# Kernel tuning notes

Hardware: AMD Instinct MI355X
Metric: run time of the kernel (lower is better)

Reference implementation:

```python
import jax, jax.numpy as jnp
import numpy as np

N, E = 50000, 600000
IN, H, O, HEADS = 14, 128, 64, 4
EPS = 1e-5


def layer_norm(x, g, b):
    m = jnp.mean(x, axis=-1, keepdims=True)
    v = jnp.mean((x - m) ** 2, axis=-1, keepdims=True)
    return (x - m) * jax.lax.rsqrt(v + EPS) * g + b


def sage_conv(x, src, dst, W_l, b_l, W_r):
    # mean aggregation of source messages at destination, then lin_l(agg)+lin_r(x)
    s = jax.ops.segment_sum(x[src], dst, num_segments=N)            # [N,H]
    cnt = jax.ops.segment_sum(jnp.ones((src.shape[0],), x.dtype), dst, num_segments=N)
    agg = s / jnp.maximum(cnt, 1.0)[:, None]
    return agg @ W_l + b_l + x @ W_r


def gat_conv(x, src, dst, W_g, att_src, att_dst, b_g):
    # PyG GATConv with add_self_loops=True, heads=4, concat=False -> head mean
    loop = jnp.arange(N, dtype=src.dtype)
    s2 = jnp.concatenate([src, loop])
    d2 = jnp.concatenate([dst, loop])
    h = (x @ W_g).reshape(N, HEADS, O)                               # [N,4,64]
    a_s = jnp.sum(h * att_src, axis=-1)                              # [N,4]
    a_d = jnp.sum(h * att_dst, axis=-1)
    e = jax.nn.leaky_relu(a_s[s2] + a_d[d2], negative_slope=0.2)     # [E+N,4]
    m = jax.ops.segment_max(e, d2, num_segments=N)
    ex = jnp.exp(e - m[d2])
    den = jax.ops.segment_sum(ex, d2, num_segments=N)
    alpha = ex / den[d2]                                             # edge softmax
    out = jax.ops.segment_sum(h[s2] * alpha[..., None], d2, num_segments=N)
    return jnp.mean(out, axis=1) + b_g                               # [N,64]


def setup_inputs() -> dict:
    key = jax.random.key(0)
    ks = jax.random.split(key, 18)
    sc = 0.05
    return {
        'x': jax.random.normal(ks[0], (N, IN), jnp.float32),
        'edge_index': jax.random.randint(ks[1], (2, E), 0, N, dtype=jnp.int64),
        'W_in': jax.random.normal(ks[2], (IN, H), jnp.float32) * sc,
        'b_in': jnp.zeros((H,), jnp.float32),
        'W1_l': jax.random.normal(ks[3], (H, H), jnp.float32) * sc,
        'b1': jnp.zeros((H,), jnp.float32),
        'W1_r': jax.random.normal(ks[4], (H, H), jnp.float32) * sc,
        'g1': jnp.ones((H,), jnp.float32),
        'be1': jnp.zeros((H,), jnp.float32),
        'W2_l': jax.random.normal(ks[5], (H, H), jnp.float32) * sc,
        'b2': jnp.zeros((H,), jnp.float32),
        'W2_r': jax.random.normal(ks[6], (H, H), jnp.float32) * sc,
        'g2': jnp.ones((H,), jnp.float32),
        'be2': jnp.zeros((H,), jnp.float32),
        'W_g': jax.random.normal(ks[7], (H, HEADS * O), jnp.float32) * sc,
        'att_src': jax.random.normal(ks[8], (HEADS, O), jnp.float32) * sc,
        'att_dst': jax.random.normal(ks[9], (HEADS, O), jnp.float32) * sc,
        'b_g': jnp.zeros((O,), jnp.float32),
        'g3': jnp.ones((O,), jnp.float32),
        'be3': jnp.zeros((O,), jnp.float32),
    }


def reference(x, edge_index, W_in, b_in, W1_l, b1, W1_r, g1, be1,
              W2_l, b2, W2_r, g2, be2, W_g, att_src, att_dst, b_g, g3, be3):
    src, dst = edge_index[0], edge_index[1]
    h = jax.nn.relu(x @ W_in + b_in)                 # input_proj + relu (dropout: eval)
    # layer 0: SAGE + LN + relu + residual
    h_res = h
    h = jax.nn.relu(layer_norm(sage_conv(h, src, dst, W1_l, b1, W1_r), g1, be1)) + h_res
    # layer 1: SAGE + LN + relu + residual
    h_res = h
    h = jax.nn.relu(layer_norm(sage_conv(h, src, dst, W2_l, b2, W2_r), g2, be2)) + h_res
    # layer 2 (last): GAT + LN, no relu/residual (shape changes H->O anyway)
    h = layer_norm(gat_conv(h, src, dst, W_g, att_src, att_dst, b_g), g3, be3)
    return h
```

## Files before the change

### kernel.cpp

```cpp
#include <hip/hip_runtime.h>
#include <math.h>

#define EPSV 1e-5f

typedef __attribute__((ext_vector_type(8))) short short8;
typedef __attribute__((ext_vector_type(4))) float f32x4;

__device__ __forceinline__ unsigned short f2b(float f) {
  union { float f; unsigned int u; } c; c.f = f;
  unsigned int u = c.u + 0x7fffu + ((c.u >> 16) & 1u);
  return (unsigned short)(u >> 16);
}
__device__ __forceinline__ float b2f(unsigned short h) {
  union { unsigned int u; float f; } c; c.u = ((unsigned int)h) << 16;
  return c.f;
}

__global__ void k_prep3(const float* __restrict__ Wl, const float* __restrict__ Wr,
                        const float* __restrict__ Wg, unsigned short* __restrict__ WlT,
                        unsigned short* __restrict__ WrT, unsigned short* __restrict__ WgT) {
  int id = blockIdx.x * 256 + threadIdx.x;
  if (id < 16384) {
    int n = id >> 7, k = id & 127;
    WlT[id] = f2b(Wl[k * 128 + n]);
  } else if (id < 32768) {
    int j = id - 16384; int n = j >> 7, k = j & 127;
    WrT[j] = f2b(Wr[k * 128 + n]);
  } else {
    int j = id - 32768; int n = j >> 7, k = j & 127;
    WgT[j] = f2b(Wg[k * 256 + n]);
  }
}
__global__ void k_prep2(const float* __restrict__ Wl, const float* __restrict__ Wr,
                        unsigned short* __restrict__ WlT, unsigned short* __restrict__ WrT) {
  int id = blockIdx.x * 256 + threadIdx.x;
  if (id < 16384) {
    int n = id >> 7, k = id & 127;
    WlT[id] = f2b(Wl[k * 128 + n]);
  } else {
    int j = id - 16384; int n = j >> 7, k = j & 127;
    WrT[j] = f2b(Wr[k * 128 + n]);
  }
}

__global__ void k_proj(const float* __restrict__ x, const float* __restrict__ W,
                       const float* __restrict__ b, unsigned short* __restrict__ h16, int nN) {
  int gid = blockIdx.x * 256 + threadIdx.x;
  if (gid >= nN * 128) return;
  int n = gid >> 7, f = gid & 127;
  const float* xr = x + n * 14;
  float acc = b[f];
#pragma unroll
  for (int k = 0; k < 14; ++k) acc = fmaf(xr[k], W[k * 128 + f], acc);
  h16[gid] = f2b(fmaxf(acc, 0.f));
}

__global__ void k_count_int(const int* __restrict__ dst, int* __restrict__ cnt, int E_) {
  int e = blockIdx.x * 256 + threadIdx.x;
  if (e < E_) atomicAdd(&cnt[dst[e]], 1);
}

__global__ void k_scan1(const int* __restrict__ cnt, int* __restrict__ incl,
                        int* __restrict__ bsum, int nN) {
  __shared__ int sh[256];
  int tid = threadIdx.x;
  int i = blockIdx.x * 256 + tid;
  int v = (i < nN) ? cnt[i] : 0;
  sh[tid] = v;
  __syncthreads();
#pragma unroll
  for (int off = 1; off < 256; off <<= 1) {
    int t = (tid >= off) ? sh[tid - off] : 0;
    __syncthreads();
    sh[tid] += t;
    __syncthreads();
  }
  if (i < nN) incl[i] = sh[tid];
  if (tid == 255) bsum[blockIdx.x] = sh[255];
}

__global__ void k_scan2(int* __restrict__ bsum, int nb) {
  __shared__ int sh[256];
  int tid = threadIdx.x;
  int v = (tid < nb) ? bsum[tid] : 0;
  sh[tid] = v;
  __syncthreads();
#pragma unroll
  for (int off = 1; off < 256; off <<= 1) {
    int t = (tid >= off) ? sh[tid - off] : 0;
    __syncthreads();
    sh[tid] += t;
    __syncthreads();
  }
  if (tid < nb) bsum[tid] = sh[tid] - v;
}

__global__ void k_scan3(const int* __restrict__ incl, const int* __restrict__ bsum,
                        const int* __restrict__ cnt, int* __restrict__ rowptr, int nN) {
  int i = blockIdx.x * 256 + threadIdx.x;
  if (i < nN) rowptr[i] = incl[i] - cnt[i] + bsum[blockIdx.x];
}

__global__ void k_fill(const int* __restrict__ src, const int* __restrict__ dst,
                       const int* __restrict__ rowptr, int* __restrict__ cursor,
                       int* __restrict__ eSrc, int E_) {
  int e = blockIdx.x * 256 + threadIdx.x;
  if (e >= E_) return;
  int d = dst[e];
  int pos = rowptr[d] + atomicAdd(&cursor[d], 1);
  eSrc[pos] = src[e];
}

__global__ void k_sage_gather16(const unsigned short* __restrict__ h16,
                                const int* __restrict__ rowptr, const int* __restrict__ cnt,
                                const int* __restrict__ eSrc,
                                unsigned short* __restrict__ agg16, int nN) {
  int t = blockIdx.x * 256 + threadIdx.x;
  int n = t >> 4;
  if (n >= nN) return;
  int sub = t & 15;
  int fo = sub * 8;
  int beg = rowptr[n], c = cnt[n];
  float a0[8], a1[8], a2[8], a3[8];
#pragma unroll
  for (int j = 0; j < 8; ++j) { a0[j] = 0.f; a1[j] = 0.f; a2[j] = 0.f; a3[j] = 0.f; }
  int i = 0;
  for (; i + 4 <= c; i += 4) {
    int s0 = eSrc[beg + i], s1 = eSrc[beg + i + 1];
    int s2 = eSrc[beg + i + 2], s3 = eSrc[beg + i + 3];
    short8 q0 = *(const short8*)(h16 + (size_t)s0 * 128 + fo);
    short8 q1 = *(const short8*)(h16 + (size_t)s1 * 128 + fo);
    short8 q2 = *(const short8*)(h16 + (size_t)s2 * 128 + fo);
    short8 q3 = *(const short8*)(h16 + (size_t)s3 * 128 + fo);
#pragma unroll
    for (int j = 0; j < 8; ++j) {
      a0[j] += b2f((unsigned short)q0[j]);
      a1[j] += b2f((unsigned short)q1[j]);
      a2[j] += b2f((unsigned short)q2[j]);
      a3[j] += b2f((unsigned short)q3[j]);
    }
  }
  for (; i < c; ++i) {
    int s = eSrc[beg + i];
    short8 q = *(const short8*)(h16 + (size_t)s * 128 + fo);
#pragma unroll
    for (int j = 0; j < 8; ++j) a0[j] += b2f((unsigned short)q[j]);
  }
  float inv = 1.f / fmaxf((float)c, 1.f);
  short8 r;
#pragma unroll
  for (int j = 0; j < 8; ++j)
    r[j] = (short)f2b(((a0[j] + a1[j]) + (a2[j] + a3[j])) * inv);
  *(short8*)(agg16 + (size_t)n * 128 + fo) = r;
}

__global__ __launch_bounds__(256)
void k_sage_mfma(const unsigned short* __restrict__ agg16,
                 const unsigned short* __restrict__ hin16,
                 const unsigned short* __restrict__ WlT,
                 const unsigned short* __restrict__ WrT,
                 const float* __restrict__ bias, const float* __restrict__ gam,
                 const float* __restrict__ bet,
                 unsigned short* __restrict__ hout16, int nN) {
  __shared__ unsigned short lA[64][136];
  __shared__ unsigned short lB[128][136];
  int tid = threadIdx.x;
  int wave = tid >> 6, lane = tid & 63;
  int cl = lane & 15, g = lane >> 4;
  int rowBase = blockIdx.x * 64;
  f32x4 acc[8];
#pragma unroll
  for (int ct = 0; ct < 8; ++ct) acc[ct] = (f32x4){0.f, 0.f, 0.f, 0.f};

  int ar = tid >> 2, ap = (tid & 3) * 32;
  int br = tid >> 1, bp = (tid & 1) * 64;

  for (int half = 0; half < 2; ++half) {
    const unsigned short* At = half ? hin16 : agg16;
    const unsigned short* Bt = half ? WrT : WlT;
    if (half) __syncthreads();
    {
      int grow = rowBase + ar;
      if (grow < nN) {
        const unsigned short* sp = At + (size_t)grow * 128 + ap;
#pragma unroll
        for (int u = 0; u < 4; ++u)
          *(short8*)&lA[ar][ap + u * 8] = *(const short8*)(sp + u * 8);
      } else {
        short8 z = {0, 0, 0, 0, 0, 0, 0, 0};
#pragma unroll
        for (int u = 0; u < 4; ++u) *(short8*)&lA[ar][ap + u * 8] = z;
      }
      const unsigned short* bsp = Bt + (size_t)br * 128 + bp;
#pragma unroll
      for (int u = 0; u < 8; ++u)
        *(short8*)&lB[br][bp + u * 8] = *(const short8*)(bsp + u * 8);
    }
    __syncthreads();
#pragma unroll
    for (int ks = 0; ks < 4; ++ks) {
      short8 a = *(const short8*)&lA[wave * 16 + cl][ks * 32 + g * 8];
#pragma unroll
      for (int ct = 0; ct < 8; ++ct) {
        short8 b = *(const short8*)&lB[ct * 16 + cl][ks * 32 + g * 8];
        acc[ct] = __builtin_amdgcn_mfma_f32_16x16x32_bf16(a, b, acc[ct], 0, 0, 0);
      }
    }
  }
  __syncthreads();

  float bcol[8], gcol[8], ecol[8];
#pragma unroll
  for (int ct = 0; ct < 8; ++ct) {
    int c = ct * 16 + cl;
    bcol[ct] = bias[c]; gcol[ct] = gam[c]; ecol[ct] = bet[c];
  }
  float v[8][4];
  float s1[4] = {0.f, 0.f, 0.f, 0.f}, s2[4] = {0.f, 0.f, 0.f, 0.f};
#pragma unroll
  for (int ct = 0; ct < 8; ++ct)
#pragma unroll
    for (int r = 0; r < 4; ++r) {
      float t = acc[ct][r] + bcol[ct];
      v[ct][r] = t;
      s1[r] += t; s2[r] += t * t;
    }
#pragma unroll
  for (int m = 1; m <= 8; m <<= 1)
#pragma unroll
    for (int r = 0; r < 4; ++r) { s1[r] += __shfl_xor(s1[r], m); s2[r] += __shfl_xor(s2[r], m); }

#pragma unroll
  for (int r = 0; r < 4; ++r) {
    float mean = s1[r] * (1.f / 128.f);
    float var = s2[r] * (1.f / 128.f) - mean * mean;
    float rstd = rsqrtf(var + EPSV);
    int grow = rowBase + wave * 16 + g * 4 + r;
    if (grow < nN) {
#pragma unroll
      for (int ct = 0; ct < 8; ++ct) {
        int c = ct * 16 + cl;
        float o = fmaxf((v[ct][r] - mean) * rstd * gcol[ct] + ecol[ct], 0.f)
                  + b2f(hin16[(size_t)grow * 128 + c]);
        hout16[(size_t)grow * 128 + c] = f2b(o);
      }
    }
  }
}

__global__ __launch_bounds__(256)
void k_gatgemm(const unsigned short* __restrict__ h16, const unsigned short* __restrict__ WgT,
               const float* __restrict__ atts, const float* __restrict__ attd,
               unsigned short* __restrict__ G16, float* __restrict__ as_,
               float* __restrict__ ad_, int nN) {
  __shared__ unsigned short lA[64][136];
  __shared__ unsigned short lB[128][136];
  int tid = threadIdx.x;
  int wave = tid >> 6, lane = tid & 63;
  int cl = lane & 15, g = lane >> 4;
  int rowBase = blockIdx.x * 64;
  int y = blockIdx.y;
  f32x4 acc[8];
#pragma unroll
  for (int ct = 0; ct < 8; ++ct) acc[ct] = (f32x4){0.f, 0.f, 0.f, 0.f};

  int ar = tid >> 2, ap = (tid & 3) * 32;
  int br = tid >> 1, bp = (tid & 1) * 64;
  {
    int grow = rowBase + ar;
    if (grow < nN) {
      const unsigned short* sp = h16 + (size_t)grow * 128 + ap;
#pragma unroll
      for (int u = 0; u < 4; ++u)
        *(short8*)&lA[ar][ap + u * 8] = *(const short8*)(sp + u * 8);
    } else {
      short8 z = {0, 0, 0, 0, 0, 0, 0, 0};
#pragma unroll
      for (int u = 0; u < 4; ++u) *(short8*)&lA[ar][ap + u * 8] = z;
    }
    const unsigned short* bsp = WgT + (size_t)(y * 128 + br) * 128 + bp;
#pragma unroll
    for (int u = 0; u < 8; ++u)
      *(short8*)&lB[br][bp + u * 8] = *(const short8*)(bsp + u * 8);
  }
  __syncthreads();
#pragma unroll
  for (int ks = 0; ks < 4; ++ks) {
    short8 a = *(const short8*)&lA[wave * 16 + cl][ks * 32 + g * 8];
#pragma unroll
    for (int ct = 0; ct < 8; ++ct) {
      short8 b = *(const short8*)&lB[ct * 16 + cl][ks * 32 + g * 8];
      acc[ct] = __builtin_amdgcn_mfma_f32_16x16x32_bf16(a, b, acc[ct], 0, 0, 0);
    }
  }

  float atr[8], adr[8];
#pragma unroll
  for (int ct = 0; ct < 8; ++ct) {
    int h = y * 2 + (ct >> 2);
    int w = (ct & 3) * 16 + cl;
    atr[ct] = atts[h * 64 + w];
    adr[ct] = attd[h * 64 + w];
  }
  float ps[2][4], pd[2][4];
#pragma unroll
  for (int hh = 0; hh < 2; ++hh)
#pragma unroll
    for (int r = 0; r < 4; ++r) { ps[hh][r] = 0.f; pd[hh][r] = 0.f; }

#pragma unroll
  for (int r = 0; r < 4; ++r) {
    int grow = rowBase + wave * 16 + g * 4 + r;
    if (grow < nN) {
      unsigned short* op = G16 + (size_t)grow * 256 + y * 128 + cl;
#pragma unroll
      for (int ct = 0; ct < 8; ++ct) op[ct * 16] = f2b(acc[ct][r]);
    }
#pragma unroll
    for (int ct = 0; ct < 8; ++ct) {
      ps[ct >> 2][r] = fmaf(acc[ct][r], atr[ct], ps[ct >> 2][r]);
      pd[ct >> 2][r] = fmaf(acc[ct][r], adr[ct], pd[ct >> 2][r]);
    }
  }
#pragma unroll
  for (int m = 1; m <= 8; m <<= 1)
#pragma unroll
    for (int hh = 0; hh < 2; ++hh)
#pragma unroll
      for (int r = 0; r < 4; ++r) {
        ps[hh][r] += __shfl_xor(ps[hh][r], m);
        pd[hh][r] += __shfl_xor(pd[hh][r], m);
      }
  if (cl == 0) {
#pragma unroll
    for (int r = 0; r < 4; ++r) {
      int grow = rowBase + wave * 16 + g * 4 + r;
      if (grow < nN) {
#pragma unroll
        for (int hh = 0; hh < 2; ++hh) {
          as_[grow * 4 + y * 2 + hh] = ps[hh][r];
          ad_[grow * 4 + y * 2 + hh] = pd[hh][r];
        }
      }
    }
  }
}

__global__ void k_gat(const unsigned short* __restrict__ G16, const int* __restrict__ rowptr,
                      const int* __restrict__ cnt, const int* __restrict__ eSrc,
                      const float* __restrict__ as_, const float* __restrict__ ad_,
                      const float* __restrict__ bg, const float* __restrict__ g3,
                      const float* __restrict__ be3, float* __restrict__ out, int nN) {
  int t = blockIdx.x * 256 + threadIdx.x;
  int n = t >> 5;
  if (n >= nN) return;
  int sub = t & 31;
  int h = sub >> 3;
  int fo = sub * 8;
  float adn = ad_[n * 4 + h];

  float e0 = as_[n * 4 + h] + adn;
  e0 = fmaxf(e0, 0.2f * e0);
  float w = __expf(e0);
  short8 q = *(const short8*)(G16 + (size_t)n * 256 + fo);
  float a0[8], a1[8], a2[8], a3[8];
#pragma unroll
  for (int j = 0; j < 8; ++j) {
    a0[j] = w * b2f((unsigned short)q[j]);
    a1[j] = 0.f; a2[j] = 0.f; a3[j] = 0.f;
  }
  float d0 = w, d1 = 0.f, d2 = 0.f, d3 = 0.f;

  int beg = rowptr[n], c = cnt[n];
  int i = 0;
  for (; i + 4 <= c; i += 4) {
    int s0 = eSrc[beg + i], s1i = eSrc[beg + i + 1];
    int s2i = eSrc[beg + i + 2], s3i = eSrc[beg + i + 3];
    float ev0 = as_[s0 * 4 + h] + adn;
    float ev1 = as_[s1i * 4 + h] + adn;
    float ev2 = as_[s2i * 4 + h] + adn;
    float ev3 = as_[s3i * 4 + h] + adn;
    ev0 = fmaxf(ev0, 0.2f * ev0); ev1 = fmaxf(ev1, 0.2f * ev1);
    ev2 = fmaxf(ev2, 0.2f * ev2); ev3 = fmaxf(ev3, 0.2f * ev3);
    float w0 = __expf(ev0), w1 = __expf(ev1), w2 = __expf(ev2), w3 = __expf(ev3);
    short8 q0 = *(const short8*)(G16 + (size_t)s0 * 256 + fo);
    short8 q1 = *(const short8*)(G16 + (size_t)s1i * 256 + fo);
    short8 q2 = *(const short8*)(G16 + (size_t)s2i * 256 + fo);
    short8 q3 = *(const short8*)(G16 + (size_t)s3i * 256 + fo);
#pragma unroll
    for (int j = 0; j < 8; ++j) {
      a0[j] = fmaf(w0, b2f((unsigned short)q0[j]), a0[j]);
      a1[j] = fmaf(w1, b2f((unsigned short)q1[j]), a1[j]);
      a2[j] = fmaf(w2, b2f((unsigned short)q2[j]), a2[j]);
      a3[j] = fmaf(w3, b2f((unsigned short)q3[j]), a3[j]);
    }
    d0 += w0; d1 += w1; d2 += w2; d3 += w3;
  }
  for (; i < c; ++i) {
    int s = eSrc[beg + i];
    float ev = as_[s * 4 + h] + adn;
    ev = fmaxf(ev, 0.2f * ev);
    w = __expf(ev);
    q = *(const short8*)(G16 + (size_t)s * 256 + fo);
#pragma unroll
    for (int j = 0; j < 8; ++j) a0[j] = fmaf(w, b2f((unsigned short)q[j]), a0[j]);
    d0 += w;
  }

  float den = (d0 + d1) + (d2 + d3);
  float inv = 1.f / den;
  float a[8];
#pragma unroll
  for (int j = 0; j < 8; ++j) a[j] = ((a0[j] + a1[j]) + (a2[j] + a3[j])) * inv;

#pragma unroll
  for (int j = 0; j < 8; ++j) {
    a[j] += __shfl_xor(a[j], 8);
    a[j] += __shfl_xor(a[j], 16);
  }
  int fb = (sub & 7) * 8;
  float v[8];
  float s1 = 0.f, s2 = 0.f;
#pragma unroll
  for (int j = 0; j < 8; ++j) {
    v[j] = a[j] * 0.25f + bg[fb + j];
    s1 += v[j]; s2 += v[j] * v[j];
  }
#pragma unroll
  for (int m = 1; m <= 4; m <<= 1) { s1 += __shfl_xor(s1, m); s2 += __shfl_xor(s2, m); }
  float mean = s1 * (1.f / 64.f);
  float var = s2 * (1.f / 64.f) - mean * mean;
  float rstd = rsqrtf(var + EPSV);
  if (sub < 8) {
    float* o = out + (size_t)n * 64 + fb;
    float4 o1, o2;
    o1.x = (v[0] - mean) * rstd * g3[fb + 0] + be3[fb + 0];
    o1.y = (v[1] - mean) * rstd * g3[fb + 1] + be3[fb + 1];
    o1.z = (v[2] - mean) * rstd * g3[fb + 2] + be3[fb + 2];
    o1.w = (v[3] - mean) * rstd * g3[fb + 3] + be3[fb + 3];
    o2.x = (v[4] - mean) * rstd * g3[fb + 4] + be3[fb + 4];
    o2.y = (v[5] - mean) * rstd * g3[fb + 5] + be3[fb + 5];
    o2.z = (v[6] - mean) * rstd * g3[fb + 6] + be3[fb + 6];
    o2.w = (v[7] - mean) * rstd * g3[fb + 7] + be3[fb + 7];
    *(float4*)o = o1;
    *(float4*)(o + 4) = o2;
  }
}

extern "C" void kernel_launch(void* const* d_in, const int* in_sizes, int n_in,
                              void* d_out, int out_size, void* d_ws, size_t ws_size,
                              hipStream_t stream) {
  const float* x    = (const float*)d_in[0];
  const int*   edge = (const int*)d_in[1];
  const float* W_in = (const float*)d_in[2];
  const float* b_in = (const float*)d_in[3];
  const float* W1_l = (const float*)d_in[4];
  const float* b1   = (const float*)d_in[5];
  const float* W1_r = (const float*)d_in[6];
  const float* g1   = (const float*)d_in[7];
  const float* be1  = (const float*)d_in[8];
  const float* W2_l = (const float*)d_in[9];
  const float* b2   = (const float*)d_in[10];
  const float* W2_r = (const float*)d_in[11];
  const float* g2   = (const float*)d_in[12];
  const float* be2  = (const float*)d_in[13];
  const float* W_g  = (const float*)d_in[14];
  const float* atts = (const float*)d_in[15];
  const float* attd = (const float*)d_in[16];
  const float* b_g  = (const float*)d_in[17];
  const float* g3   = (const float*)d_in[18];
  const float* be3  = (const float*)d_in[19];

  const int nN = in_sizes[0] / 14;
  const int E_ = in_sizes[1] / 2;
  const int* src = edge;
  const int* dst = edge + E_;

  char* W = (char*)d_ws;
  unsigned short* hA16  = (unsigned short*)W; W += (size_t)nN * 128 * 2;
  unsigned short* hB16  = (unsigned short*)W; W += (size_t)nN * 128 * 2;
  unsigned short* agg16 = (unsigned short*)W; W += (size_t)nN * 128 * 2;
  unsigned short* G16   = (unsigned short*)W; W += (size_t)nN * 256 * 2;
  unsigned short* WlT   = (unsigned short*)W; W += 16384 * 2;
  unsigned short* WrT   = (unsigned short*)W; W += 16384 * 2;
  unsigned short* WgT   = (unsigned short*)W; W += 32768 * 2;
  float* AS_ = (float*)W;                W += (size_t)nN * 4 * 4;
  float* AD_ = (float*)W;                W += (size_t)nN * 4 * 4;
  int* cntI   = (int*)W;                 W += (size_t)nN * 4;
  int* rowptr = (int*)W;                 W += (size_t)nN * 4;
  int* cursor = (int*)W;                 W += (size_t)nN * 4;
  int* incl   = (int*)W;                 W += (size_t)nN * 4;
  int* bsum   = (int*)W;                 W += 1024 * 4;
  int* eSrc   = (int*)W;

  const int SB = (nN + 255) / 256;
  const int NB = (nN + 63) / 64;

  hipMemsetAsync(cntI, 0, (size_t)nN * sizeof(int), stream);
  hipMemsetAsync(cursor, 0, (size_t)nN * sizeof(int), stream);

  k_count_int<<<(E_ + 255) / 256, 256, 0, stream>>>(dst, cntI, E_);
  k_scan1<<<SB, 256, 0, stream>>>(cntI, incl, bsum, nN);
  k_scan2<<<1, 256, 0, stream>>>(bsum, SB);
  k_scan3<<<SB, 256, 0, stream>>>(incl, bsum, cntI, rowptr, nN);
  k_fill<<<(E_ + 255) / 256, 256, 0, stream>>>(src, dst, rowptr, cursor, eSrc, E_);

  k_prep3<<<256, 256, 0, stream>>>(W1_l, W1_r, W_g, WlT, WrT, WgT);
  k_proj<<<(nN * 128 + 255) / 256, 256, 0, stream>>>(x, W_in, b_in, hA16, nN);

  k_sage_gather16<<<(nN * 16 + 255) / 256, 256, 0, stream>>>(hA16, rowptr, cntI, eSrc, agg16, nN);
  k_sage_mfma<<<NB, 256, 0, stream>>>(agg16, hA16, WlT, WrT, b1, g1, be1, hB16, nN);

  k_prep2<<<128, 256, 0, stream>>>(W2_l, W2_r, WlT, WrT);
  k_sage_gather16<<<(nN * 16 + 255) / 256, 256, 0, stream>>>(hB16, rowptr, cntI, eSrc, agg16, nN);
  k_sage_mfma<<<NB, 256, 0, stream>>>(agg16, hB16, WlT, WrT, b2, g2, be2, hA16, nN);

  k_gatgemm<<<dim3(NB, 2), 256, 0, stream>>>(hA16, WgT, atts, attd, G16, AS_, AD_, nN);
  k_gat<<<(nN * 32 + 255) / 256, 256, 0, stream>>>(G16, rowptr, cntI, eSrc, AS_, AD_, b_g, g3, be3, (float*)d_out, nN);
}
```

Before: 267.7 us.

## Quantize gathered node features to per-row uint8 for SAGE and GAT gathers

```diff
diff --git a/kernel.cpp b/kernel.cpp
--- a/kernel.cpp
+++ b/kernel.cpp
@@ -14,6 +14,9 @@
 __device__ __forceinline__ float b2f(unsigned short h) {
   union { unsigned int u; float f; } c; c.u = ((unsigned int)h) << 16;
   return c.f;
+}
+__device__ __forceinline__ float ub(unsigned int w, int j) {
+  return (float)((w >> (8 * j)) & 0xffu);
 }
 
 __global__ void k_prep3(const float* __restrict__ Wl, const float* __restrict__ Wr,
@@ -44,15 +47,34 @@
 }
 
 __global__ void k_proj(const float* __restrict__ x, const float* __restrict__ W,
-                       const float* __restrict__ b, unsigned short* __restrict__ h16, int nN) {
-  int gid = blockIdx.x * 256 + threadIdx.x;
-  if (gid >= nN * 128) return;
-  int n = gid >> 7, f = gid & 127;
-  const float* xr = x + n * 14;
-  float acc = b[f];
-#pragma unroll
-  for (int k = 0; k < 14; ++k) acc = fmaf(xr[k], W[k * 128 + f], acc);
-  h16[gid] = f2b(fmaxf(acc, 0.f));
+                       const float* __restrict__ b, unsigned short* __restrict__ h16,
+                       unsigned char* __restrict__ h8, float2* __restrict__ hmeta, int nN) {
+  int t = blockIdx.x * 256 + threadIdx.x;
+  int n = t >> 6;
+  if (n >= nN) return;
+  int lane = t & 63;
+  const float* xr = x + (size_t)n * 14;
+  float acc0 = b[lane], acc1 = b[lane + 64];
+#pragma unroll
+  for (int k = 0; k < 14; ++k) {
+    float xv = xr[k];
+    acc0 = fmaf(xv, W[k * 128 + lane], acc0);
+    acc1 = fmaf(xv, W[k * 128 + lane + 64], acc1);
+  }
+  float o0 = fmaxf(acc0, 0.f), o1 = fmaxf(acc1, 0.f);
+  h16[(size_t)n * 128 + lane] = f2b(o0);
+  h16[(size_t)n * 128 + lane + 64] = f2b(o1);
+  float rmin = fminf(o0, o1), rmax = fmaxf(o0, o1);
+#pragma unroll
+  for (int m = 1; m <= 32; m <<= 1) {
+    rmin = fminf(rmin, __shfl_xor(rmin, m));
+    rmax = fmaxf(rmax, __shfl_xor(rmax, m));
+  }
+  float scale = (rmax - rmin) * (1.f / 255.f);
+  float invq = (rmax > rmin) ? 255.f / (rmax - rmin) : 0.f;
+  h8[(size_t)n * 128 + lane] = (unsigned char)(int)rintf((o0 - rmin) * invq);
+  h8[(size_t)n * 128 + lane + 64] = (unsigned char)(int)rintf((o1 - rmin) * invq);
+  if (lane == 0) hmeta[n] = make_float2(scale, rmin);
 }
 
 __global__ void k_count_int(const int* __restrict__ dst, int* __restrict__ cnt, int E_) {
@@ -111,10 +133,11 @@
   eSrc[pos] = src[e];
 }
 
-__global__ void k_sage_gather16(const unsigned short* __restrict__ h16,
-                                const int* __restrict__ rowptr, const int* __restrict__ cnt,
-                                const int* __restrict__ eSrc,
-                                unsigned short* __restrict__ agg16, int nN) {
+__global__ void k_sage_gather8(const unsigned char* __restrict__ h8,
+                               const float2* __restrict__ hmeta,
+                               const int* __restrict__ rowptr, const int* __restrict__ cnt,
+                               const int* __restrict__ eSrc,
+                               unsigned short* __restrict__ agg16, int nN) {
   int t = blockIdx.x * 256 + threadIdx.x;
   int n = t >> 4;
   if (n >= nN) return;
@@ -124,33 +147,46 @@
   float a0[8], a1[8], a2[8], a3[8];
 #pragma unroll
   for (int j = 0; j < 8; ++j) { a0[j] = 0.f; a1[j] = 0.f; a2[j] = 0.f; a3[j] = 0.f; }
+  float m0 = 0.f, m1 = 0.f, m2 = 0.f, m3 = 0.f;
   int i = 0;
   for (; i + 4 <= c; i += 4) {
     int s0 = eSrc[beg + i], s1 = eSrc[beg + i + 1];
     int s2 = eSrc[beg + i + 2], s3 = eSrc[beg + i + 3];
-    short8 q0 = *(const short8*)(h16 + (size_t)s0 * 128 + fo);
-    short8 q1 = *(const short8*)(h16 + (size_t)s1 * 128 + fo);
-    short8 q2 = *(const short8*)(h16 + (size_t)s2 * 128 + fo);
-    short8 q3 = *(const short8*)(h16 + (size_t)s3 * 128 + fo);
-#pragma unroll
-    for (int j = 0; j < 8; ++j) {
-      a0[j] += b2f((unsigned short)q0[j]);
-      a1[j] += b2f((unsigned short)q1[j]);
-      a2[j] += b2f((unsigned short)q2[j]);
-      a3[j] += b2f((unsigned short)q3[j]);
-    }
+    float2 t0 = hmeta[s0], t1 = hmeta[s1], t2 = hmeta[s2], t3 = hmeta[s3];
+    uint2 p0 = *(const uint2*)(h8 + (size_t)s0 * 128 + fo);
+    uint2 p1 = *(const uint2*)(h8 + (size_t)s1 * 128 + fo);
+    uint2 p2 = *(const uint2*)(h8 + (size_t)s2 * 128 + fo);
+    uint2 p3 = *(const uint2*)(h8 + (size_t)s3 * 128 + fo);
+#pragma unroll
+    for (int j = 0; j < 4; ++j) {
+      a0[j] = fmaf(t0.x, ub(p0.x, j), a0[j]);
+      a1[j] = fmaf(t1.x, ub(p1.x, j), a1[j]);
+      a2[j] = fmaf(t2.x, ub(p2.x, j), a2[j]);
+      a3[j] = fmaf(t3.x, ub(p3.x, j), a3[j]);
+      a0[j + 4] = fmaf(t0.x, ub(p0.y, j), a0[j + 4]);
+      a1[j + 4] = fmaf(t1.x, ub(p1.y, j), a1[j + 4]);
+      a2[j + 4] = fmaf(t2.x, ub(p2.y, j), a2[j + 4]);
+      a3[j + 4] = fmaf(t3.x, ub(p3.y, j), a3[j + 4]);
+    }
+    m0 += t0.y; m1 += t1.y; m2 += t2.y; m3 += t3.y;
   }
   for (; i < c; ++i) {
     int s = eSrc[beg + i];
-    short8 q = *(const short8*)(h16 + (size_t)s * 128 + fo);
-#pragma unroll
-    for (int j = 0; j < 8; ++j) a0[j] += b2f((unsigned short)q[j]);
-  }
+    float2 tm = hmeta[s];
+    uint2 p = *(const uint2*)(h8 + (size_t)s * 128 + fo);
+#pragma unroll
+    for (int j = 0; j < 4; ++j) {
+      a0[j] = fmaf(tm.x, ub(p.x, j), a0[j]);
+      a0[j + 4] = fmaf(tm.x, ub(p.y, j), a0[j + 4]);
+    }
+    m0 += tm.y;
+  }
+  float mm = (m0 + m1) + (m2 + m3);
   float inv = 1.f / fmaxf((float)c, 1.f);
   short8 r;
 #pragma unroll
   for (int j = 0; j < 8; ++j)
-    r[j] = (short)f2b(((a0[j] + a1[j]) + (a2[j] + a3[j])) * inv);
+    r[j] = (short)f2b((((a0[j] + a1[j]) + (a2[j] + a3[j])) + mm) * inv);
   *(short8*)(agg16 + (size_t)n * 128 + fo) = r;
 }
 
@@ -161,7 +197,9 @@
                  const unsigned short* __restrict__ WrT,
                  const float* __restrict__ bias, const float* __restrict__ gam,
                  const float* __restrict__ bet,
-                 unsigned short* __restrict__ hout16, int nN) {
+                 unsigned short* __restrict__ hout16,
+                 unsigned char* __restrict__ hout8, float2* __restrict__ hmeta_o,
+                 int quant, int nN) {
   __shared__ unsigned short lA[64][136];
   __shared__ unsigned short lB[128][136];
   int tid = threadIdx.x;
@@ -237,12 +275,31 @@
     float rstd = rsqrtf(var + EPSV);
     int grow = rowBase + wave * 16 + g * 4 + r;
     if (grow < nN) {
+      float o8v[8];
+      float rmin = 1e30f, rmax = -1e30f;
 #pragma unroll
       for (int ct = 0; ct < 8; ++ct) {
         int c = ct * 16 + cl;
         float o = fmaxf((v[ct][r] - mean) * rstd * gcol[ct] + ecol[ct], 0.f)
                   + b2f(hin16[(size_t)grow * 128 + c]);
+        o8v[ct] = o;
+        rmin = fminf(rmin, o); rmax = fmaxf(rmax, o);
         hout16[(size_t)grow * 128 + c] = f2b(o);
+      }
+      if (quant) {
+#pragma unroll
+        for (int m = 1; m <= 8; m <<= 1) {
+          rmin = fminf(rmin, __shfl_xor(rmin, m));
+          rmax = fmaxf(rmax, __shfl_xor(rmax, m));
+        }
+        float scale = (rmax - rmin) * (1.f / 255.f);
+        float invq = (rmax > rmin) ? 255.f / (rmax - rmin) : 0.f;
+#pragma unroll
+        for (int ct = 0; ct < 8; ++ct) {
+          int c = ct * 16 + cl;
+          hout8[(size_t)grow * 128 + c] = (unsigned char)(int)rintf((o8v[ct] - rmin) * invq);
+        }
+        if (cl == 0) hmeta_o[grow] = make_float2(scale, rmin);
       }
     }
   }
@@ -251,8 +308,8 @@
 __global__ __launch_bounds__(256)
 void k_gatgemm(const unsigned short* __restrict__ h16, const unsigned short* __restrict__ WgT,
                const float* __restrict__ atts, const float* __restrict__ attd,
-               unsigned short* __restrict__ G16, float* __restrict__ as_,
-               float* __restrict__ ad_, int nN) {
+               unsigned char* __restrict__ G8, float2* __restrict__ Gmeta,
+               float* __restrict__ as_, float* __restrict__ ad_, int nN) {
   __shared__ unsigned short lA[64][136];
   __shared__ unsigned short lB[128][136];
   int tid = threadIdx.x;
@@ -311,10 +368,24 @@
 #pragma unroll
   for (int r = 0; r < 4; ++r) {
     int grow = rowBase + wave * 16 + g * 4 + r;
+    float rmin = 1e30f, rmax = -1e30f;
+#pragma unroll
+    for (int ct = 0; ct < 8; ++ct) {
+      rmin = fminf(rmin, acc[ct][r]); rmax = fmaxf(rmax, acc[ct][r]);
+    }
+#pragma unroll
+    for (int m = 1; m <= 8; m <<= 1) {
+      rmin = fminf(rmin, __shfl_xor(rmin, m));
+      rmax = fmaxf(rmax, __shfl_xor(rmax, m));
+    }
+    float scale = (rmax - rmin) * (1.f / 255.f);
+    float invq = (rmax > rmin) ? 255.f / (rmax - rmin) : 0.f;
     if (grow < nN) {
-      unsigned short* op = G16 + (size_t)grow * 256 + y * 128 + cl;
-#pragma unroll
-      for (int ct = 0; ct < 8; ++ct) op[ct * 16] = f2b(acc[ct][r]);
+      unsigned char* op = G8 + (size_t)grow * 256 + y * 128 + cl;
+#pragma unroll
+      for (int ct = 0; ct < 8; ++ct)
+        op[ct * 16] = (unsigned char)(int)rintf((acc[ct][r] - rmin) * invq);
+      if (cl == 0) Gmeta[grow * 2 + y] = make_float2(scale, rmin);
     }
 #pragma unroll
     for (int ct = 0; ct < 8; ++ct) {
@@ -346,8 +417,9 @@
   }
 }
 
-__global__ void k_gat(const unsigned short* __restrict__ G16, const int* __restrict__ rowptr,
-                      const int* __restrict__ cnt, const int* __restrict__ eSrc,
+__global__ void k_gat(const unsigned char* __restrict__ G8, const float2* __restrict__ Gmeta,
+                      const int* __restrict__ rowptr, const int* __restrict__ cnt,
+                      const int* __restrict__ eSrc,
                       const float* __restrict__ as_, const float* __restrict__ ad_,
                       const float* __restrict__ bg, const float* __restrict__ g3,
                       const float* __restrict__ be3, float* __restrict__ out, int nN) {
@@ -356,19 +428,26 @@
   if (n >= nN) return;
   int sub = t & 31;
   int h = sub >> 3;
+  int yy = sub >> 4;
   int fo = sub * 8;
   float adn = ad_[n * 4 + h];
 
   float e0 = as_[n * 4 + h] + adn;
   e0 = fmaxf(e0, 0.2f * e0);
   float w = __expf(e0);
-  short8 q = *(const short8*)(G16 + (size_t)n * 256 + fo);
+  float2 mts = Gmeta[n * 2 + yy];
+  uint2 p = *(const uint2*)(G8 + (size_t)n * 256 + fo);
+  float ws = w * mts.x;
   float a0[8], a1[8], a2[8], a3[8];
 #pragma unroll
-  for (int j = 0; j < 8; ++j) {
-    a0[j] = w * b2f((unsigned short)q[j]);
-    a1[j] = 0.f; a2[j] = 0.f; a3[j] = 0.f;
-  }
+  for (int j = 0; j < 4; ++j) {
+    a0[j] = ws * ub(p.x, j);
+    a0[j + 4] = ws * ub(p.y, j);
+    a1[j] = 0.f; a1[j + 4] = 0.f;
+    a2[j] = 0.f; a2[j + 4] = 0.f;
+    a3[j] = 0.f; a3[j + 4] = 0.f;
+  }
+  float m0 = w * mts.y, m1 = 0.f, m2 = 0.f, m3 = 0.f;
   float d0 = w, d1 = 0.f, d2 = 0.f, d3 = 0.f;
 
   int beg = rowptr[n], c = cnt[n];
@@ -383,17 +462,26 @@
     ev0 = fmaxf(ev0, 0.2f * ev0); ev1 = fmaxf(ev1, 0.2f * ev1);
     ev2 = fmaxf(ev2, 0.2f * ev2); ev3 = fmaxf(ev3, 0.2f * ev3);
     float w0 = __expf(ev0), w1 = __expf(ev1), w2 = __expf(ev2), w3 = __expf(ev3);
-    short8 q0 = *(const short8*)(G16 + (size_t)s0 * 256 + fo);
-    short8 q1 = *(const short8*)(G16 + (size_t)s1i * 256 + fo);
-    short8 q2 = *(const short8*)(G16 + (size_t)s2i * 256 + fo);
-    short8 q3 = *(const short8*)(G16 + (size_t)s3i * 256 + fo);
-#pragma unroll
-    for (int j = 0; j < 8; ++j) {
-      a0[j] = fmaf(w0, b2f((unsigned short)q0[j]), a0[j]);
-      a1[j] = fmaf(w1, b2f((unsigned short)q1[j]), a1[j]);
-      a2[j] = fmaf(w2, b2f((unsigned short)q2[j]), a2[j]);
-      a3[j] = fmaf(w3, b2f((unsigned short)q3[j]), a3[j]);
-    }
+    float2 t0 = Gmeta[s0 * 2 + yy], t1 = Gmeta[s1i * 2 + yy];
+    float2 t2 = Gmeta[s2i * 2 + yy], t3 = Gmeta[s3i * 2 + yy];
+    uint2 p0 = *(const uint2*)(G8 + (size_t)s0 * 256 + fo);
+    uint2 p1 = *(const uint2*)(G8 + (size_t)s1i * 256 + fo);
+    uint2 p2 = *(const uint2*)(G8 + (size_t)s2i * 256 + fo);
+    uint2 p3 = *(const uint2*)(G8 + (size_t)s3i * 256 + fo);
+    float ws0 = w0 * t0.x, ws1 = w1 * t1.x, ws2 = w2 * t2.x, ws3 = w3 * t3.x;
+#pragma unroll
+    for (int j = 0; j < 4; ++j) {
+      a0[j] = fmaf(ws0, ub(p0.x, j), a0[j]);
+      a1[j] = fmaf(ws1, ub(p1.x, j), a1[j]);
+      a2[j] = fmaf(ws2, ub(p2.x, j), a2[j]);
+      a3[j] = fmaf(ws3, ub(p3.x, j), a3[j]);
+      a0[j + 4] = fmaf(ws0, ub(p0.y, j), a0[j + 4]);
+      a1[j + 4] = fmaf(ws1, ub(p1.y, j), a1[j + 4]);
+      a2[j + 4] = fmaf(ws2, ub(p2.y, j), a2[j + 4]);
+      a3[j + 4] = fmaf(ws3, ub(p3.y, j), a3[j + 4]);
+    }
+    m0 = fmaf(w0, t0.y, m0); m1 = fmaf(w1, t1.y, m1);
+    m2 = fmaf(w2, t2.y, m2); m3 = fmaf(w3, t3.y, m3);
     d0 += w0; d1 += w1; d2 += w2; d3 += w3;
   }
   for (; i < c; ++i) {
@@ -401,17 +489,25 @@
     float ev = as_[s * 4 + h] + adn;
     ev = fmaxf(ev, 0.2f * ev);
     w = __expf(ev);
-    q = *(const short8*)(G16 + (size_t)s * 256 + fo);
-#pragma unroll
-    for (int j = 0; j < 8; ++j) a0[j] = fmaf(w, b2f((unsigned short)q[j]), a0[j]);
+    float2 tm = Gmeta[s * 2 + yy];
+    p = *(const uint2*)(G8 + (size_t)s * 256 + fo);
+    float wsx = w * tm.x;
+#pragma unroll
+    for (int j = 0; j < 4; ++j) {
+      a0[j] = fmaf(wsx, ub(p.x, j), a0[j]);
+      a0[j + 4] = fmaf(wsx, ub(p.y, j), a0[j + 4]);
+    }
+    m0 = fmaf(w, tm.y, m0);
     d0 += w;
   }
 
   float den = (d0 + d1) + (d2 + d3);
+  float mm = (m0 + m1) + (m2 + m3);
   float inv = 1.f / den;
   float a[8];
 #pragma unroll
-  for (int j = 0; j < 8; ++j) a[j] = ((a0[j] + a1[j]) + (a2[j] + a3[j])) * inv;
+  for (int j = 0; j < 8; ++j)
+    a[j] = (((a0[j] + a1[j]) + (a2[j] + a3[j])) + mm) * inv;
 
 #pragma unroll
   for (int j = 0; j < 8; ++j) {
@@ -480,18 +576,23 @@
   unsigned short* hA16  = (unsigned short*)W; W += (size_t)nN * 128 * 2;
   unsigned short* hB16  = (unsigned short*)W; W += (size_t)nN * 128 * 2;
   unsigned short* agg16 = (unsigned short*)W; W += (size_t)nN * 128 * 2;
-  unsigned short* G16   = (unsigned short*)W; W += (size_t)nN * 256 * 2;
   unsigned short* WlT   = (unsigned short*)W; W += 16384 * 2;
   unsigned short* WrT   = (unsigned short*)W; W += 16384 * 2;
   unsigned short* WgT   = (unsigned short*)W; W += 32768 * 2;
   float* AS_ = (float*)W;                W += (size_t)nN * 4 * 4;
   float* AD_ = (float*)W;                W += (size_t)nN * 4 * 4;
+  float2* metaA = (float2*)W;            W += (size_t)nN * 8;
+  float2* metaB = (float2*)W;            W += (size_t)nN * 8;
+  float2* Gmeta = (float2*)W;            W += (size_t)nN * 2 * 8;
   int* cntI   = (int*)W;                 W += (size_t)nN * 4;
   int* rowptr = (int*)W;                 W += (size_t)nN * 4;
   int* cursor = (int*)W;                 W += (size_t)nN * 4;
   int* incl   = (int*)W;                 W += (size_t)nN * 4;
   int* bsum   = (int*)W;                 W += 1024 * 4;
-  int* eSrc   = (int*)W;
+  int* eSrc   = (int*)W;                 W += (size_t)E_ * 4;
+  unsigned char* h8A = (unsigned char*)W; W += (size_t)nN * 128;
+  unsigned char* h8B = (unsigned char*)W; W += (size_t)nN * 128;
+  unsigned char* G8  = (unsigned char*)W; W += (size_t)nN * 256;
 
   const int SB = (nN + 255) / 256;
   const int NB = (nN + 63) / 64;
@@ -506,15 +607,15 @@
   k_fill<<<(E_ + 255) / 256, 256, 0, stream>>>(src, dst, rowptr, cursor, eSrc, E_);
 
   k_prep3<<<256, 256, 0, stream>>>(W1_l, W1_r, W_g, WlT, WrT, WgT);
-  k_proj<<<(nN * 128 + 255) / 256, 256, 0, stream>>>(x, W_in, b_in, hA16, nN);
-
-  k_sage_gather16<<<(nN * 16 + 255) / 256, 256, 0, stream>>>(hA16, rowptr, cntI, eSrc, agg16, nN);
-  k_sage_mfma<<<NB, 256, 0, stream>>>(agg16, hA16, WlT, WrT, b1, g1, be1, hB16, nN);
+  k_proj<<<(nN * 64 + 255) / 256, 256, 0, stream>>>(x, W_in, b_in, hA16, h8A, metaA, nN);
+
+  k_sage_gather8<<<(nN * 16 + 255) / 256, 256, 0, stream>>>(h8A, metaA, rowptr, cntI, eSrc, agg16, nN);
+  k_sage_mfma<<<NB, 256, 0, stream>>>(agg16, hA16, WlT, WrT, b1, g1, be1, hB16, h8B, metaB, 1, nN);
 
   k_prep2<<<128, 256, 0, stream>>>(W2_l, W2_r, WlT, WrT);
-  k_sage_gather16<<<(nN * 16 + 255) / 256, 256, 0, stream>>>(hB16, rowptr, cntI, eSrc, agg16, nN);
-  k_sage_mfma<<<NB, 256, 0, stream>>>(agg16, hB16, WlT, WrT, b2, g2, be2, hA16, nN);
-
-  k_gatgemm<<<dim3(NB, 2), 256, 0, stream>>>(hA16, WgT, atts, attd, G16, AS_, AD_, nN);
-  k_gat<<<(nN * 32 + 255) / 256, 256, 0, stream>>>(G16, rowptr, cntI, eSrc, AS_, AD_, b_g, g3, be3, (float*)d_out, nN);
-}
+  k_sage_gather8<<<(nN * 16 + 255) / 256, 256, 0, stream>>>(h8B, metaB, rowptr, cntI, eSrc, agg16, nN);
+  k_sage_mfma<<<NB, 256, 0, stream>>>(agg16, hB16, WlT, WrT, b2, g2, be2, hA16, h8A, metaA, 0, nN);
+
+  k_gatgemm<<<dim3(NB, 2), 256, 0, stream>>>(hA16, WgT, atts, attd, G8, Gmeta, AS_, AD_, nN);
+  k_gat<<<(nN * 32 + 255) / 256, 256, 0, stream>>>(G8, Gmeta, rowptr, cntI, eSrc, AS_, AD_, b_g, g3, be3, (float*)d_out, nN);
+}
```

Result: no change. 265.5 us (-0.8%).
